# Performance work log

Hardware: AMD Instinct MI355X
Metric: run time of the kernel (lower is better)

## Reference

```python
import math
import jax, jax.numpy as jnp
import numpy as np

EMBED_DIM = 768
NUM_HEADS = 12
HEAD_DIM = EMBED_DIM // NUM_HEADS
NUM_BUCKETS = 32
MAX_DISTANCE = 128
B, S = 8, 1024


def setup_inputs() -> dict:
    key = jax.random.key(0)
    ks = jax.random.split(key, 16)
    sc = 0.02
    d = {
        "query": jax.random.normal(ks[0], (B, S, EMBED_DIM), jnp.float32),
        "Wq": jax.random.normal(ks[1], (EMBED_DIM, EMBED_DIM), jnp.float32) * sc,
        "bq": jnp.zeros((EMBED_DIM,), jnp.float32),
        "Wk": jax.random.normal(ks[2], (EMBED_DIM, EMBED_DIM), jnp.float32) * sc,
        "bk": jnp.zeros((EMBED_DIM,), jnp.float32),
        "Wv": jax.random.normal(ks[3], (EMBED_DIM, EMBED_DIM), jnp.float32) * sc,
        "bv": jnp.zeros((EMBED_DIM,), jnp.float32),
        "Wo": jax.random.normal(ks[4], (EMBED_DIM, EMBED_DIM), jnp.float32) * sc,
        "bo": jnp.zeros((EMBED_DIM,), jnp.float32),
        "rel_embed": jax.random.normal(ks[5], (NUM_BUCKETS, NUM_HEADS), jnp.float32) * sc,
        "gru_W": jax.random.normal(ks[6], (HEAD_DIM, 8), jnp.float32) * sc,
        "gru_b": jnp.zeros((8,), jnp.float32),
        "gru_const": jnp.ones((1, NUM_HEADS, 1, 1), jnp.float32),
    }
    return d


def _rel_pos_bias(rel_embed, seq_len):
    # bidirectional T5-style bucketing, matching WavLM._relative_positions_bucket
    ctx = jnp.arange(seq_len)[:, None]
    mem = jnp.arange(seq_len)[None, :]
    rp = mem - ctx  # [S, S]
    nb = NUM_BUCKETS // 2
    buckets = (rp > 0).astype(jnp.int32) * nb
    arp = jnp.abs(rp)
    max_exact = nb // 2
    is_small = arp < max_exact
    # truncation toward zero == astype for positive values; clamp to avoid log(0)
    large = max_exact + (
        jnp.log(jnp.maximum(arp, 1).astype(jnp.float32) / max_exact)
        / math.log(MAX_DISTANCE / max_exact)
        * (nb - max_exact)
    ).astype(jnp.int32)
    large = jnp.minimum(large, nb - 1)
    buckets = buckets + jnp.where(is_small, arp, large)
    # embedding lookup -> [S, S, H] -> [H, S, S]
    return rel_embed[buckets].transpose(2, 0, 1)


def reference(query, Wq, bq, Wk, bk, Wv, bv, Wo, bo, rel_embed, gru_W, gru_b, gru_const):
    b, s, e = query.shape
    h, d = NUM_HEADS, HEAD_DIM
    pos_bias = _rel_pos_bias(rel_embed, s)  # [H, S, S]

    # GRU-style gate computed from raw query, per head
    ql = query.reshape(b, s, h, d).transpose(0, 2, 1, 3)  # [B, H, S, D]
    g = jax.nn.sigmoid((ql @ gru_W + gru_b).reshape(b, h, s, 2, 4).sum(-1))  # [B,H,S,2]
    gate_a = g[..., 0:1]
    gate_b = g[..., 1:2]
    gate = gate_a * (gate_b * gru_const - 1.0) + 2.0  # [B, H, S, 1]
    attn_mask = gate * pos_bias[None]  # [B, H, S, S]

    scale = d ** (-0.5)
    q = (query @ Wq + bq).reshape(b, s, h, d).transpose(0, 2, 1, 3) * scale
    k = (query @ Wk + bk).reshape(b, s, h, d).transpose(0, 2, 1, 3)
    v = (query @ Wv + bv).reshape(b, s, h, d).transpose(0, 2, 1, 3)

    scores = jnp.einsum("bhqd,bhkd->bhqk", q, k) + attn_mask
    w = jax.nn.softmax(scores, axis=-1)  # max-subtraction in torch is a no-op math-wise
    out = jnp.einsum("bhqk,bhkd->bhqd", w, v)
    out = out.transpose(0, 2, 1, 3).reshape(b, s, h * d)
    return out @ Wo + bo
```

## Files before the change

kernel.cpp:

```cpp
#include <hip/hip_runtime.h>
#include <hip/hip_bf16.h>
#include <math.h>

#define EMBED 768
#define NH 12
#define HD 64
#define SEQ 1024
#define BATCH 8
#define NROWS (BATCH * SEQ)
#define LOG2E 1.44269504088896340736f

typedef __attribute__((ext_vector_type(4))) float f32x4;
typedef __attribute__((ext_vector_type(8))) short short8;
typedef __attribute__((ext_vector_type(8))) _Float16 half8;
typedef unsigned short u16;

__device__ __forceinline__ u16 f2bf(float x) {
    union { float f; unsigned u; } v; v.f = x;
    unsigned r = v.u + 0x7fff + ((v.u >> 16) & 1);
    return (u16)(r >> 16);
}
__device__ __forceinline__ void split2h(float x, u16& hi, u16& lo) {
    _Float16 h = (_Float16)x;
    _Float16 l = (_Float16)(x - (float)h);
    union { _Float16 f; u16 u; } a, b;
    a.f = h; b.f = l;
    hi = a.u; lo = b.u;
}
__device__ __forceinline__ u16 f2h(float x) {
    union { _Float16 f; u16 u; } a; a.f = (_Float16)x; return a.u;
}
__device__ __forceinline__ unsigned pkbf(float a, float b) {
    union { __hip_bfloat162 v; unsigned u; } cv;
    cv.v = __float22bfloat162_rn(make_float2(a, b));
    return cv.u;
}
__device__ __forceinline__ void gll16(const void* g, void* l) {
    __builtin_amdgcn_global_load_lds(
        (const __attribute__((address_space(1))) unsigned int*)g,
        (__attribute__((address_space(3))) unsigned int*)l,
        16, 0, 0);
}
__device__ __forceinline__ void pipe_barrier() {
    asm volatile("s_waitcnt vmcnt(0)" ::: "memory");
    __builtin_amdgcn_s_barrier();
    asm volatile("" ::: "memory");
}

__global__ void bias_table_kernel(const float* __restrict__ rel_embed,
                                  float* __restrict__ bt)
{
    int idx = blockIdx.x * 256 + threadIdx.x;
    const int total = NH * 2047;
    if (idx >= total) return;
    int h    = idx / 2047;
    int dpos = idx - h * 2047;
    int rp   = dpos - 1023;
    int bucket = (rp > 0) ? 16 : 0;
    int arp = rp < 0 ? -rp : rp;
    if (arp < 8) {
        bucket += arp;
    } else {
        double v = log((double)arp / 8.0) / log(16.0) * 8.0;
        int l = 8 + (int)v;
        if (l > 15) l = 15;
        bucket += l;
    }
    bt[idx] = rel_embed[bucket * NH + h] * LOG2E;
}

__global__ void gate_kernel(const float* __restrict__ query,
                            const float* __restrict__ gru_W,
                            const float* __restrict__ gru_b,
                            const float* __restrict__ gru_c,
                            float* __restrict__ gate)
{
    int idx = blockIdx.x * 256 + threadIdx.x;
    if (idx >= BATCH * NH * SEQ) return;
    int s  = idx & (SEQ - 1);
    int bh = idx >> 10;
    int h  = bh % NH;
    int b  = bh / NH;

    const float* x = query + ((size_t)(b * SEQ + s) * EMBED + h * HD);
    float z[8] = {0.f, 0.f, 0.f, 0.f, 0.f, 0.f, 0.f, 0.f};
    for (int d = 0; d < HD; ++d) {
        float xv = x[d];
        const float* wrow = gru_W + d * 8;
        #pragma unroll
        for (int c = 0; c < 8; ++c) z[c] += xv * wrow[c];
    }
    float s0 = (z[0] + gru_b[0]) + (z[1] + gru_b[1]) + (z[2] + gru_b[2]) + (z[3] + gru_b[3]);
    float s1 = (z[4] + gru_b[4]) + (z[5] + gru_b[5]) + (z[6] + gru_b[6]) + (z[7] + gru_b[7]);
    float g0 = 1.f / (1.f + expf(-s0));
    float g1 = 1.f / (1.f + expf(-s1));
    gate[idx] = g0 * (g1 * gru_c[h] - 1.f) + 2.f;
}

__global__ __launch_bounds__(256)
void convertA_h(const float* __restrict__ A, u16* __restrict__ Ah,
                u16* __restrict__ Al)
{
    int idx = (blockIdx.x * 256 + threadIdx.x) * 4;
    float4 v = *(const float4*)(A + idx);
    ushort4 h, l;
    split2h(v.x, h.x, l.x); split2h(v.y, h.y, l.y);
    split2h(v.z, h.z, l.z); split2h(v.w, h.w, l.w);
    *(ushort4*)(Ah + idx) = h;
    *(ushort4*)(Al + idx) = l;
}

__global__ __launch_bounds__(256)
void convertWT4(const float* __restrict__ W0, const float* __restrict__ W1,
                const float* __restrict__ W2, const float* __restrict__ W3,
                u16* __restrict__ T0, u16* __restrict__ T1,
                u16* __restrict__ T2, u16* __restrict__ T3)
{
    __shared__ float tile[32][33];
    const float* W = (blockIdx.z == 0) ? W0 : (blockIdx.z == 1) ? W1
                   : (blockIdx.z == 2) ? W2 : W3;
    u16* WT        = (blockIdx.z == 0) ? T0 : (blockIdx.z == 1) ? T1
                   : (blockIdx.z == 2) ? T2 : T3;
    int t  = threadIdx.x;
    int k0 = blockIdx.y * 32, n0 = blockIdx.x * 32;
    int r = t >> 3, c = (t & 7) * 4;
    float4 v = *(const float4*)&W[(size_t)(k0 + r) * EMBED + n0 + c];
    tile[r][c] = v.x; tile[r][c + 1] = v.y; tile[r][c + 2] = v.z; tile[r][c + 3] = v.w;
    __syncthreads();
    int n = t >> 3, ks = (t & 7) * 4;
    ushort4 h;
    h.x = f2h(tile[ks    ][n]);
    h.y = f2h(tile[ks + 1][n]);
    h.z = f2h(tile[ks + 2][n]);
    h.w = f2h(tile[ks + 3][n]);
    *(ushort4*)&WT[(size_t)(n0 + n) * EMBED + k0 + ks] = h;
}

__global__ __launch_bounds__(256, 3)
void gemm_qkv_p(const u16* __restrict__ Ah, const u16* __restrict__ Al,
                const u16* __restrict__ WqT, const u16* __restrict__ WkT,
                const u16* __restrict__ WvT,
                const float* __restrict__ bq, const float* __restrict__ bk,
                const float* __restrict__ bv,
                u16* __restrict__ Qb, u16* __restrict__ Kb, u16* __restrict__ VT,
                float qscale)
{
    __shared__ u16 Bs[2][3][128 * 32];

    const int t    = threadIdx.x;
    const int lane = t & 63;
    const int wid  = t >> 6;
    const int L    = lane & 15;
    const int quad = lane >> 4;
    const int row0 = blockIdx.y * 32;
    const int col0 = blockIdx.x * 128;
    const int wm   = (wid >> 1) * 16;
    const int wn   = (wid & 1) * 64;

    f32x4 accQ[4], accK[4], accV[4];
    #pragma unroll
    for (int nt = 0; nt < 4; ++nt) {
        accQ[nt] = (f32x4){0.f, 0.f, 0.f, 0.f};
        accK[nt] = (f32x4){0.f, 0.f, 0.f, 0.f};
        accV[nt] = (f32x4){0.f, 0.f, 0.f, 0.f};
    }

    const int rB = t >> 2;
    const int cB = (t & 3) ^ (rB & 3);
    const size_t bo0 = (size_t)(col0 + rB) * EMBED + 8 * cB;
    const size_t bo1 = (size_t)(col0 + 64 + rB) * EMBED + 8 * cB;

    const u16* ApH = Ah + (size_t)(row0 + wm + L) * EMBED + quad * 8;
    const u16* ApL = Al + (size_t)(row0 + wm + L) * EMBED + quad * 8;

    const int swz = 8 * (quad ^ (L & 3));

    {
        char* base = (char*)Bs + wid * 1024;
        gll16(WqT + bo0, base);             gll16(WqT + bo1, base + 4096);
        gll16(WkT + bo0, base + 8192);      gll16(WkT + bo1, base + 12288);
        gll16(WvT + bo0, base + 16384);     gll16(WvT + bo1, base + 20480);
    }
    half8 ah = *(const half8*)ApH;
    half8 al = *(const half8*)ApL;

    int cur = 0;
    for (int k0 = 0; k0 < EMBED; k0 += 32, cur ^= 1) {
        pipe_barrier();

        half8 ahn, aln;
        if (k0 + 32 < EMBED) {
            char* base = (char*)Bs + (cur ^ 1) * 24576 + wid * 1024;
            gll16(WqT + bo0 + k0 + 32, base);         gll16(WqT + bo1 + k0 + 32, base + 4096);
            gll16(WkT + bo0 + k0 + 32, base + 8192);  gll16(WkT + bo1 + k0 + 32, base + 12288);
            gll16(WvT + bo0 + k0 + 32, base + 16384); gll16(WvT + bo1 + k0 + 32, base + 20480);
            ahn = *(const half8*)(ApH + k0 + 32);
            aln = *(const half8*)(ApL + k0 + 32);
        }

        const u16* Bq = &Bs[cur][0][0];
        const u16* Bk = &Bs[cur][1][0];
        const u16* Bv = &Bs[cur][2][0];
        #pragma unroll
        for (int nt = 0; nt < 4; ++nt) {
            const int boff = (wn + nt * 16 + L) * 32 + swz;
            half8 b0 = *(const half8*)&Bq[boff];
            accQ[nt] = __builtin_amdgcn_mfma_f32_16x16x32_f16(ah, b0, accQ[nt], 0, 0, 0);
            accQ[nt] = __builtin_amdgcn_mfma_f32_16x16x32_f16(al, b0, accQ[nt], 0, 0, 0);
            half8 b1 = *(const half8*)&Bk[boff];
            accK[nt] = __builtin_amdgcn_mfma_f32_16x16x32_f16(ah, b1, accK[nt], 0, 0, 0);
            accK[nt] = __builtin_amdgcn_mfma_f32_16x16x32_f16(al, b1, accK[nt], 0, 0, 0);
            half8 b2 = *(const half8*)&Bv[boff];
            accV[nt] = __builtin_amdgcn_mfma_f32_16x16x32_f16(ah, b2, accV[nt], 0, 0, 0);
            accV[nt] = __builtin_amdgcn_mfma_f32_16x16x32_f16(al, b2, accV[nt], 0, 0, 0);
        }
        ah = ahn; al = aln;
    }

    float bq4[4], bk4[4], bv4[4];
    #pragma unroll
    for (int nt = 0; nt < 4; ++nt) {
        int n = col0 + wn + nt * 16 + L;
        bq4[nt] = bq[n]; bk4[nt] = bk[n]; bv4[nt] = bv[n];
    }

    const int rowa = row0 + wm + quad * 4;
    #pragma unroll
    for (int r = 0; r < 4; ++r) {
        size_t base = (size_t)(rowa + r) * EMBED + col0 + wn + L;
        #pragma unroll
        for (int nt = 0; nt < 4; ++nt) {
            Qb[base + nt * 16] = f2bf((accQ[nt][r] + bq4[nt]) * qscale);
            Kb[base + nt * 16] = f2bf(accK[nt][r] + bk4[nt]);
        }
    }
    {
        int b_  = rowa >> 10;
        int s0_ = rowa & 1023;
        #pragma unroll
        for (int nt = 0; nt < 4; ++nt) {
            int n = col0 + wn + nt * 16 + L;
            int hh = n >> 6, dd = n & 63;
            ushort4 pk;
            pk.x = f2bf(accV[nt][0] + bv4[nt]);
            pk.y = f2bf(accV[nt][1] + bv4[nt]);
            pk.z = f2bf(accV[nt][2] + bv4[nt]);
            pk.w = f2bf(accV[nt][3] + bv4[nt]);
            *(ushort4*)&VT[((size_t)(b_ * NH + hh) * HD + dd) * SEQ + s0_] = pk;
        }
    }
}

__global__ __launch_bounds__(256, 3)
void gemm_out_p(const u16* __restrict__ Ah, const u16* __restrict__ Al,
                const u16* __restrict__ BT, const float* __restrict__ bias,
                float* __restrict__ C)
{
    __shared__ u16 Bs[2][128 * 32];

    const int t    = threadIdx.x;
    const int lane = t & 63;
    const int wid  = t >> 6;
    const int L    = lane & 15;
    const int quad = lane >> 4;
    const int row0 = blockIdx.y * 64;
    const int col0 = blockIdx.x * 128;
    const int wm   = (wid >> 1) * 32;
    const int wn   = (wid & 1) * 64;

    f32x4 acc[2][4];
    #pragma unroll
    for (int mt = 0; mt < 2; ++mt)
        #pragma unroll
        for (int nt = 0; nt < 4; ++nt) acc[mt][nt] = (f32x4){0.f, 0.f, 0.f, 0.f};

    const int rB = t >> 2;
    const int cB = (t & 3) ^ (rB & 3);
    const size_t bo0 = (size_t)(col0 + rB) * EMBED + 8 * cB;
    const size_t bo1 = (size_t)(col0 + 64 + rB) * EMBED + 8 * cB;

    const u16* ApH[2]; const u16* ApL[2];
    #pragma unroll
    for (int mt = 0; mt < 2; ++mt) {
        ApH[mt] = Ah + (size_t)(row0 + wm + mt * 16 + L) * EMBED + quad * 8;
        ApL[mt] = Al + (size_t)(row0 + wm + mt * 16 + L) * EMBED + quad * 8;
    }

    const int swz = 8 * (quad ^ (L & 3));

    {
        char* base = (char*)Bs + wid * 1024;
        gll16(BT + bo0, base);
        gll16(BT + bo1, base + 4096);
    }
    half8 ah[2], al[2];
    #pragma unroll
    for (int mt = 0; mt < 2; ++mt) {
        ah[mt] = *(const half8*)ApH[mt];
        al[mt] = *(const half8*)ApL[mt];
    }

    int cur = 0;
    for (int k0 = 0; k0 < EMBED; k0 += 32, cur ^= 1) {
        pipe_barrier();

        half8 ahn[2], aln[2];
        if (k0 + 32 < EMBED) {
            char* base = (char*)Bs + (cur ^ 1) * 8192 + wid * 1024;
            gll16(BT + bo0 + k0 + 32, base);
            gll16(BT + bo1 + k0 + 32, base + 4096);
            #pragma unroll
            for (int mt = 0; mt < 2; ++mt) {
                ahn[mt] = *(const half8*)(ApH[mt] + k0 + 32);
                aln[mt] = *(const half8*)(ApL[mt] + k0 + 32);
            }
        }

        const u16* B = &Bs[cur][0];
        #pragma unroll
        for (int nt = 0; nt < 4; ++nt) {
            half8 b = *(const half8*)&B[(wn + nt * 16 + L) * 32 + swz];
            #pragma unroll
            for (int mt = 0; mt < 2; ++mt) {
                acc[mt][nt] = __builtin_amdgcn_mfma_f32_16x16x32_f16(ah[mt], b, acc[mt][nt], 0, 0, 0);
                acc[mt][nt] = __builtin_amdgcn_mfma_f32_16x16x32_f16(al[mt], b, acc[mt][nt], 0, 0, 0);
            }
        }
        #pragma unroll
        for (int mt = 0; mt < 2; ++mt) { ah[mt] = ahn[mt]; al[mt] = aln[mt]; }
    }

    float b4[4];
    #pragma unroll
    for (int nt = 0; nt < 4; ++nt) b4[nt] = bias[col0 + wn + nt * 16 + L];
    #pragma unroll
    for (int mt = 0; mt < 2; ++mt)
        #pragma unroll
        for (int r = 0; r < 4; ++r) {
            size_t base = (size_t)(row0 + wm + mt * 16 + quad * 4 + r) * EMBED + col0 + wn + L;
            #pragma unroll
            for (int nt = 0; nt < 4; ++nt)
                C[base + nt * 16] = acc[mt][nt][r] + b4[nt];
        }
}

__global__ __launch_bounds__(256)
void attn_mfma3(const u16* __restrict__ Qg, const u16* __restrict__ Kg,
                const u16* __restrict__ VTg, const float* __restrict__ gate,
                const float* __restrict__ bias_tab,
                u16* __restrict__ Oh, u16* __restrict__ Ol)
{
    __shared__ float2   btP[2047];
    __shared__ u16      Klds[64 * 64];
    __shared__ u16      Vlds[64 * 64];
    __shared__ unsigned PB[4][32 * 20];

    const int t    = threadIdx.x;
    const int lane = t & 63;
    const int wid  = t >> 6;
    const int L    = lane & 15;
    const int quad = lane >> 4;

    const int bh = blockIdx.y;
    const int b  = bh / NH;
    const int h  = bh % NH;
    const int qw = blockIdx.x * 128 + wid * 32;

    for (int i = t; i < 2047; i += 256) {
        float a  = bias_tab[h * 2047 + i];
        float nb = (i < 2046) ? bias_tab[h * 2047 + i + 1] : 0.f;
        btP[i] = make_float2(a, nb);
    }

    short8 qf[2][2];
    int   qabs[2];
    float g2[2];
    #pragma unroll
    for (int qt = 0; qt < 2; ++qt) {
        qabs[qt] = qw + qt * 16 + L;
        g2[qt]   = gate[(size_t)bh * SEQ + qabs[qt]];
        const u16* qp = Qg + ((size_t)(b * SEQ + qabs[qt]) * EMBED + h * HD + quad * 8);
        qf[qt][0] = *(const short8*)qp;
        qf[qt][1] = *(const short8*)(qp + 32);
    }

    float lac[2] = {0.f, 0.f};
    f32x4 o[4][2];
    #pragma unroll
    for (int dt = 0; dt < 4; ++dt)
        #pragma unroll
        for (int qt = 0; qt < 2; ++qt) o[dt][qt] = (f32x4){0.f, 0.f, 0.f, 0.f};

    const int k_a = t >> 3, c_a = (t & 7) ^ (k_a & 7);
    const u16* gK0 = Kg + ((size_t)(b * SEQ + k_a) * EMBED + h * HD + 8 * c_a);
    const u16* gK1 = Kg + ((size_t)(b * SEQ + 32 + k_a) * EMBED + h * HD + 8 * c_a);
    char* lK0 = (char*)Klds + wid * 1024;
    char* lK1 = (char*)Klds + 4096 + wid * 1024;

    const int d_a = t >> 3, cv_a = (t & 7) ^ (d_a & 7);
    const u16* gV0 = VTg + ((size_t)(bh * HD + d_a) * SEQ + 8 * cv_a);
    const u16* gV1 = VTg + ((size_t)(bh * HD + 32 + d_a) * SEQ + 8 * cv_a);
    char* lV0 = (char*)Vlds + wid * 1024;
    char* lV1 = (char*)Vlds + 4096 + wid * 1024;

    unsigned* PBw = PB[wid];

    for (int k0 = 0; k0 < SEQ; k0 += 64) {
        __syncthreads();
        gll16(gK0 + (size_t)k0 * EMBED, lK0);
        gll16(gK1 + (size_t)k0 * EMBED, lK1);
        gll16(gV0 + k0, lV0);
        gll16(gV1 + k0, lV1);
        __syncthreads();

        f32x4 st[4][2];
        #pragma unroll
        for (int kt = 0; kt < 4; ++kt)
            #pragma unroll
            for (int qt = 0; qt < 2; ++qt) st[kt][qt] = (f32x4){0.f, 0.f, 0.f, 0.f};
        #pragma unroll
        for (int c = 0; c < 2; ++c) {
            #pragma unroll
            for (int kt = 0; kt < 4; ++kt) {
                int krow = kt * 16 + L;
                short8 kf = *(const short8*)&Klds[krow * 64 + 8 * ((c * 4 + quad) ^ (krow & 7))];
                st[kt][0] = __builtin_amdgcn_mfma_f32_16x16x32_bf16(kf, qf[0][c], st[kt][0], 0, 0, 0);
                st[kt][1] = __builtin_amdgcn_mfma_f32_16x16x32_bf16(kf, qf[1][c], st[kt][1], 0, 0, 0);
            }
        }

        #pragma unroll
        for (int c = 0; c < 2; ++c) {
            #pragma unroll
            for (int kt2 = 0; kt2 < 2; ++kt2) {
                int kt = c * 2 + kt2;
                #pragma unroll
                for (int qt = 0; qt < 2; ++qt) {
                    int bidx = k0 + kt * 16 + quad * 4 - qabs[qt] + 1023;
                    float2 u = btP[bidx];
                    float2 v = btP[bidx + 2];
                    float p0 = __builtin_amdgcn_exp2f(st[kt][qt][0] + g2[qt] * u.x);
                    float p1 = __builtin_amdgcn_exp2f(st[kt][qt][1] + g2[qt] * u.y);
                    float p2 = __builtin_amdgcn_exp2f(st[kt][qt][2] + g2[qt] * v.x);
                    float p3 = __builtin_amdgcn_exp2f(st[kt][qt][3] + g2[qt] * v.y);
                    lac[qt] += (p0 + p1) + (p2 + p3);
                    uint2 w;
                    w.x = pkbf(p0, p1);
                    w.y = pkbf(p2, p3);
                    *(uint2*)&PBw[(qt * 16 + L) * 20 + kt2 * 8 + quad * 2] = w;
                }
            }
            short8 pb[2];
            #pragma unroll
            for (int qt = 0; qt < 2; ++qt) {
                union { uint4 u4; short8 v; } w;
                w.u4 = *(const uint4*)&PBw[(qt * 16 + L) * 20 + quad * 4];
                pb[qt] = w.v;
            }
            #pragma unroll
            for (int dt = 0; dt < 4; ++dt) {
                int drow = dt * 16 + L;
                short8 vf = *(const short8*)&Vlds[drow * 64 + 8 * ((c * 4 + quad) ^ (drow & 7))];
                o[dt][0] = __builtin_amdgcn_mfma_f32_16x16x32_bf16(vf, pb[0], o[dt][0], 0, 0, 0);
                o[dt][1] = __builtin_amdgcn_mfma_f32_16x16x32_bf16(vf, pb[1], o[dt][1], 0, 0, 0);
            }
        }
    }

    #pragma unroll
    for (int qt = 0; qt < 2; ++qt) {
        lac[qt] += __shfl_xor(lac[qt], 16);
        lac[qt] += __shfl_xor(lac[qt], 32);
    }
    #pragma unroll
    for (int qt = 0; qt < 2; ++qt) {
        float inv = 1.f / lac[qt];
        #pragma unroll
        for (int dt = 0; dt < 4; ++dt) {
            ushort4 h4, l4;
            split2h(o[dt][qt][0] * inv, h4.x, l4.x);
            split2h(o[dt][qt][1] * inv, h4.y, l4.y);
            split2h(o[dt][qt][2] * inv, h4.z, l4.z);
            split2h(o[dt][qt][3] * inv, h4.w, l4.w);
            size_t base = (size_t)(b * SEQ + qabs[qt]) * EMBED + h * HD + dt * 16 + quad * 4;
            *(ushort4*)&Oh[base] = h4;
            *(ushort4*)&Ol[base] = l4;
        }
    }
}

extern "C" void kernel_launch(void* const* d_in, const int* in_sizes, int n_in,
                              void* d_out, int out_size, void* d_ws, size_t ws_size,
                              hipStream_t stream)
{
    (void)in_sizes; (void)n_in; (void)out_size; (void)ws_size;
    const float* query = (const float*)d_in[0];
    const float* Wq    = (const float*)d_in[1];
    const float* bq    = (const float*)d_in[2];
    const float* Wk    = (const float*)d_in[3];
    const float* bk    = (const float*)d_in[4];
    const float* Wv    = (const float*)d_in[5];
    const float* bv    = (const float*)d_in[6];
    const float* Wo    = (const float*)d_in[7];
    const float* bo    = (const float*)d_in[8];
    const float* rel   = (const float*)d_in[9];
    const float* gruW  = (const float*)d_in[10];
    const float* gruB  = (const float*)d_in[11];
    const float* gruC  = (const float*)d_in[12];
    float* out = (float*)d_out;

    const size_t NE = (size_t)NROWS * EMBED;
    const size_t WN = (size_t)EMBED * EMBED;
    u16* ws   = (u16*)d_ws;
    u16* Ah   = ws;
    u16* Al   = Ah + NE;
    u16* WqT  = Al + NE;
    u16* WkT  = WqT + WN;
    u16* WvT  = WkT + WN;
    u16* WoT  = WvT + WN;
    u16* Qb   = WoT + WN;
    u16* Kb   = Qb + NE;
    u16* VT   = Kb + NE;
    u16* Ohb  = VT + NE;
    u16* Olb  = Ohb + NE;
    float* gate = (float*)(Olb + NE);
    float* bt   = gate + (size_t)BATCH * NH * SEQ;

    bias_table_kernel<<<(NH * 2047 + 255) / 256, 256, 0, stream>>>(rel, bt);
    gate_kernel<<<(BATCH * NH * SEQ + 255) / 256, 256, 0, stream>>>(query, gruW, gruB, gruC, gate);

    convertA_h<<<NE / 1024, 256, 0, stream>>>(query, Ah, Al);
    convertWT4<<<dim3(EMBED / 32, EMBED / 32, 4), 256, 0, stream>>>(
        Wq, Wk, Wv, Wo, WqT, WkT, WvT, WoT);

    dim3 gq(EMBED / 128, NROWS / 32);
    gemm_qkv_p<<<gq, 256, 0, stream>>>(Ah, Al, WqT, WkT, WvT, bq, bk, bv,
                                       Qb, Kb, VT, 0.125f * LOG2E);

    attn_mfma3<<<dim3(SEQ / 128, BATCH * NH), 256, 0, stream>>>(Qb, Kb, VT, gate, bt, Ohb, Olb);

    dim3 go(EMBED / 128, NROWS / 64);
    gemm_out_p<<<go, 256, 0, stream>>>(Ohb, Olb, WoT, bo, out);
}
```

Measured before the change: 302.8 us.

## Drop split-fp16 low parts and enlarge QKV GEMM tile to 64 rows

Replaces the hi/lo split-fp16 emulation of fp32 with a single fp16 operand for the activations in both the QKV and output projections. This halves the MFMA count and the A-operand traffic, and removes the low-part buffers and their writes from the conversion and attention kernels. The QKV GEMM now computes 64 rows per block (two M-subtiles per wave) so each staged weight tile is reused more. The LDS swizzle pattern also changes. Accuracy drops to plain fp16 inputs, which risks exceeding the tolerance.

Result: faster. 245.3 us (-19.0%).

```diff
diff --git a/kernel.cpp b/kernel.cpp
--- a/kernel.cpp
+++ b/kernel.cpp
@@ -19,13 +19,6 @@
     union { float f; unsigned u; } v; v.f = x;
     unsigned r = v.u + 0x7fff + ((v.u >> 16) & 1);
     return (u16)(r >> 16);
-}
-__device__ __forceinline__ void split2h(float x, u16& hi, u16& lo) {
-    _Float16 h = (_Float16)x;
-    _Float16 l = (_Float16)(x - (float)h);
-    union { _Float16 f; u16 u; } a, b;
-    a.f = h; b.f = l;
-    hi = a.u; lo = b.u;
 }
 __device__ __forceinline__ u16 f2h(float x) {
     union { _Float16 f; u16 u; } a; a.f = (_Float16)x; return a.u;
@@ -98,16 +91,13 @@
 }
 
 __global__ __launch_bounds__(256)
-void convertA_h(const float* __restrict__ A, u16* __restrict__ Ah,
-                u16* __restrict__ Al)
+void convertA1(const float* __restrict__ A, u16* __restrict__ Ah)
 {
     int idx = (blockIdx.x * 256 + threadIdx.x) * 4;
     float4 v = *(const float4*)(A + idx);
-    ushort4 h, l;
-    split2h(v.x, h.x, l.x); split2h(v.y, h.y, l.y);
-    split2h(v.z, h.z, l.z); split2h(v.w, h.w, l.w);
+    ushort4 h;
+    h.x = f2h(v.x); h.y = f2h(v.y); h.z = f2h(v.z); h.w = f2h(v.w);
     *(ushort4*)(Ah + idx) = h;
-    *(ushort4*)(Al + idx) = l;
 }
 
 __global__ __launch_bounds__(256)
@@ -137,7 +127,7 @@
 }
 
 __global__ __launch_bounds__(256, 3)
-void gemm_qkv_p(const u16* __restrict__ Ah, const u16* __restrict__ Al,
+void gemm_qkv_s(const u16* __restrict__ Ah,
                 const u16* __restrict__ WqT, const u16* __restrict__ WkT,
                 const u16* __restrict__ WvT,
                 const float* __restrict__ bq, const float* __restrict__ bk,
@@ -146,117 +136,6 @@
                 float qscale)
 {
     __shared__ u16 Bs[2][3][128 * 32];
-
-    const int t    = threadIdx.x;
-    const int lane = t & 63;
-    const int wid  = t >> 6;
-    const int L    = lane & 15;
-    const int quad = lane >> 4;
-    const int row0 = blockIdx.y * 32;
-    const int col0 = blockIdx.x * 128;
-    const int wm   = (wid >> 1) * 16;
-    const int wn   = (wid & 1) * 64;
-
-    f32x4 accQ[4], accK[4], accV[4];
-    #pragma unroll
-    for (int nt = 0; nt < 4; ++nt) {
-        accQ[nt] = (f32x4){0.f, 0.f, 0.f, 0.f};
-        accK[nt] = (f32x4){0.f, 0.f, 0.f, 0.f};
-        accV[nt] = (f32x4){0.f, 0.f, 0.f, 0.f};
-    }
-
-    const int rB = t >> 2;
-    const int cB = (t & 3) ^ (rB & 3);
-    const size_t bo0 = (size_t)(col0 + rB) * EMBED + 8 * cB;
-    const size_t bo1 = (size_t)(col0 + 64 + rB) * EMBED + 8 * cB;
-
-    const u16* ApH = Ah + (size_t)(row0 + wm + L) * EMBED + quad * 8;
-    const u16* ApL = Al + (size_t)(row0 + wm + L) * EMBED + quad * 8;
-
-    const int swz = 8 * (quad ^ (L & 3));
-
-    {
-        char* base = (char*)Bs + wid * 1024;
-        gll16(WqT + bo0, base);             gll16(WqT + bo1, base + 4096);
-        gll16(WkT + bo0, base + 8192);      gll16(WkT + bo1, base + 12288);
-        gll16(WvT + bo0, base + 16384);     gll16(WvT + bo1, base + 20480);
-    }
-    half8 ah = *(const half8*)ApH;
-    half8 al = *(const half8*)ApL;
-
-    int cur = 0;
-    for (int k0 = 0; k0 < EMBED; k0 += 32, cur ^= 1) {
-        pipe_barrier();
-
-        half8 ahn, aln;
-        if (k0 + 32 < EMBED) {
-            char* base = (char*)Bs + (cur ^ 1) * 24576 + wid * 1024;
-            gll16(WqT + bo0 + k0 + 32, base);         gll16(WqT + bo1 + k0 + 32, base + 4096);
-            gll16(WkT + bo0 + k0 + 32, base + 8192);  gll16(WkT + bo1 + k0 + 32, base + 12288);
-            gll16(WvT + bo0 + k0 + 32, base + 16384); gll16(WvT + bo1 + k0 + 32, base + 20480);
-            ahn = *(const half8*)(ApH + k0 + 32);
-            aln = *(const half8*)(ApL + k0 + 32);
-        }
-
-        const u16* Bq = &Bs[cur][0][0];
-        const u16* Bk = &Bs[cur][1][0];
-        const u16* Bv = &Bs[cur][2][0];
-        #pragma unroll
-        for (int nt = 0; nt < 4; ++nt) {
-            const int boff = (wn + nt * 16 + L) * 32 + swz;
-            half8 b0 = *(const half8*)&Bq[boff];
-            accQ[nt] = __builtin_amdgcn_mfma_f32_16x16x32_f16(ah, b0, accQ[nt], 0, 0, 0);
-            accQ[nt] = __builtin_amdgcn_mfma_f32_16x16x32_f16(al, b0, accQ[nt], 0, 0, 0);
-            half8 b1 = *(const half8*)&Bk[boff];
-            accK[nt] = __builtin_amdgcn_mfma_f32_16x16x32_f16(ah, b1, accK[nt], 0, 0, 0);
-            accK[nt] = __builtin_amdgcn_mfma_f32_16x16x32_f16(al, b1, accK[nt], 0, 0, 0);
-            half8 b2 = *(const half8*)&Bv[boff];
-            accV[nt] = __builtin_amdgcn_mfma_f32_16x16x32_f16(ah, b2, accV[nt], 0, 0, 0);
-            accV[nt] = __builtin_amdgcn_mfma_f32_16x16x32_f16(al, b2, accV[nt], 0, 0, 0);
-        }
-        ah = ahn; al = aln;
-    }
-
-    float bq4[4], bk4[4], bv4[4];
-    #pragma unroll
-    for (int nt = 0; nt < 4; ++nt) {
-        int n = col0 + wn + nt * 16 + L;
-        bq4[nt] = bq[n]; bk4[nt] = bk[n]; bv4[nt] = bv[n];
-    }
-
-    const int rowa = row0 + wm + quad * 4;
-    #pragma unroll
-    for (int r = 0; r < 4; ++r) {
-        size_t base = (size_t)(rowa + r) * EMBED + col0 + wn + L;
-        #pragma unroll
-        for (int nt = 0; nt < 4; ++nt) {
-            Qb[base + nt * 16] = f2bf((accQ[nt][r] + bq4[nt]) * qscale);
-            Kb[base + nt * 16] = f2bf(accK[nt][r] + bk4[nt]);
-        }
-    }
-    {
-        int b_  = rowa >> 10;
-        int s0_ = rowa & 1023;
-        #pragma unroll
-        for (int nt = 0; nt < 4; ++nt) {
-            int n = col0 + wn + nt * 16 + L;
-            int hh = n >> 6, dd = n & 63;
-            ushort4 pk;
-            pk.x = f2bf(accV[nt][0] + bv4[nt]);
-            pk.y = f2bf(accV[nt][1] + bv4[nt]);
-            pk.z = f2bf(accV[nt][2] + bv4[nt]);
-            pk.w = f2bf(accV[nt][3] + bv4[nt]);
-            *(ushort4*)&VT[((size_t)(b_ * NH + hh) * HD + dd) * SEQ + s0_] = pk;
-        }
-    }
-}
-
-__global__ __launch_bounds__(256, 3)
-void gemm_out_p(const u16* __restrict__ Ah, const u16* __restrict__ Al,
-                const u16* __restrict__ BT, const float* __restrict__ bias,
-                float* __restrict__ C)
-{
-    __shared__ u16 Bs[2][128 * 32];
 
     const int t    = threadIdx.x;
     const int lane = t & 63;
@@ -268,52 +147,163 @@
     const int wm   = (wid >> 1) * 32;
     const int wn   = (wid & 1) * 64;
 
-    f32x4 acc[2][4];
+    f32x4 accQ[2][4], accK[2][4], accV[2][4];
     #pragma unroll
     for (int mt = 0; mt < 2; ++mt)
         #pragma unroll
-        for (int nt = 0; nt < 4; ++nt) acc[mt][nt] = (f32x4){0.f, 0.f, 0.f, 0.f};
+        for (int nt = 0; nt < 4; ++nt) {
+            accQ[mt][nt] = (f32x4){0.f, 0.f, 0.f, 0.f};
+            accK[mt][nt] = (f32x4){0.f, 0.f, 0.f, 0.f};
+            accV[mt][nt] = (f32x4){0.f, 0.f, 0.f, 0.f};
+        }
 
     const int rB = t >> 2;
-    const int cB = (t & 3) ^ (rB & 3);
+    const int cB = (t & 3) ^ ((rB >> 1) & 3);
     const size_t bo0 = (size_t)(col0 + rB) * EMBED + 8 * cB;
     const size_t bo1 = (size_t)(col0 + 64 + rB) * EMBED + 8 * cB;
 
-    const u16* ApH[2]; const u16* ApL[2];
+    const u16* ApH[2];
+    #pragma unroll
+    for (int mt = 0; mt < 2; ++mt)
+        ApH[mt] = Ah + (size_t)(row0 + wm + mt * 16 + L) * EMBED + quad * 8;
+
+    const int swz = 8 * (quad ^ ((L >> 1) & 3));
+
+    {
+        char* base = (char*)Bs + wid * 1024;
+        gll16(WqT + bo0, base);             gll16(WqT + bo1, base + 4096);
+        gll16(WkT + bo0, base + 8192);      gll16(WkT + bo1, base + 12288);
+        gll16(WvT + bo0, base + 16384);     gll16(WvT + bo1, base + 20480);
+    }
+    half8 ah[2];
+    #pragma unroll
+    for (int mt = 0; mt < 2; ++mt) ah[mt] = *(const half8*)ApH[mt];
+
+    int cur = 0;
+    for (int k0 = 0; k0 < EMBED; k0 += 32, cur ^= 1) {
+        pipe_barrier();
+
+        half8 ahn[2];
+        if (k0 + 32 < EMBED) {
+            char* base = (char*)Bs + (cur ^ 1) * 24576 + wid * 1024;
+            gll16(WqT + bo0 + k0 + 32, base);         gll16(WqT + bo1 + k0 + 32, base + 4096);
+            gll16(WkT + bo0 + k0 + 32, base + 8192);  gll16(WkT + bo1 + k0 + 32, base + 12288);
+            gll16(WvT + bo0 + k0 + 32, base + 16384); gll16(WvT + bo1 + k0 + 32, base + 20480);
+            #pragma unroll
+            for (int mt = 0; mt < 2; ++mt) ahn[mt] = *(const half8*)(ApH[mt] + k0 + 32);
+        }
+
+        const u16* Bq = &Bs[cur][0][0];
+        const u16* Bk = &Bs[cur][1][0];
+        const u16* Bv = &Bs[cur][2][0];
+        #pragma unroll
+        for (int nt = 0; nt < 4; ++nt) {
+            const int boff = (wn + nt * 16 + L) * 32 + swz;
+            half8 b0 = *(const half8*)&Bq[boff];
+            accQ[0][nt] = __builtin_amdgcn_mfma_f32_16x16x32_f16(ah[0], b0, accQ[0][nt], 0, 0, 0);
+            accQ[1][nt] = __builtin_amdgcn_mfma_f32_16x16x32_f16(ah[1], b0, accQ[1][nt], 0, 0, 0);
+            half8 b1 = *(const half8*)&Bk[boff];
+            accK[0][nt] = __builtin_amdgcn_mfma_f32_16x16x32_f16(ah[0], b1, accK[0][nt], 0, 0, 0);
+            accK[1][nt] = __builtin_amdgcn_mfma_f32_16x16x32_f16(ah[1], b1, accK[1][nt], 0, 0, 0);
+            half8 b2 = *(const half8*)&Bv[boff];
+            accV[0][nt] = __builtin_amdgcn_mfma_f32_16x16x32_f16(ah[0], b2, accV[0][nt], 0, 0, 0);
+            accV[1][nt] = __builtin_amdgcn_mfma_f32_16x16x32_f16(ah[1], b2, accV[1][nt], 0, 0, 0);
+        }
+        #pragma unroll
+        for (int mt = 0; mt < 2; ++mt) ah[mt] = ahn[mt];
+    }
+
+    float bq4[4], bk4[4], bv4[4];
+    #pragma unroll
+    for (int nt = 0; nt < 4; ++nt) {
+        int n = col0 + wn + nt * 16 + L;
+        bq4[nt] = bq[n]; bk4[nt] = bk[n]; bv4[nt] = bv[n];
+    }
+
     #pragma unroll
     for (int mt = 0; mt < 2; ++mt) {
+        const int rowa = row0 + wm + mt * 16 + quad * 4;
+        #pragma unroll
+        for (int r = 0; r < 4; ++r) {
+            size_t base = (size_t)(rowa + r) * EMBED + col0 + wn + L;
+            #pragma unroll
+            for (int nt = 0; nt < 4; ++nt) {
+                Qb[base + nt * 16] = f2bf((accQ[mt][nt][r] + bq4[nt]) * qscale);
+                Kb[base + nt * 16] = f2bf(accK[mt][nt][r] + bk4[nt]);
+            }
+        }
+        {
+            int b_  = rowa >> 10;
+            int s0_ = rowa & 1023;
+            #pragma unroll
+            for (int nt = 0; nt < 4; ++nt) {
+                int n = col0 + wn + nt * 16 + L;
+                int hh = n >> 6, dd = n & 63;
+                ushort4 pk;
+                pk.x = f2bf(accV[mt][nt][0] + bv4[nt]);
+                pk.y = f2bf(accV[mt][nt][1] + bv4[nt]);
+                pk.z = f2bf(accV[mt][nt][2] + bv4[nt]);
+                pk.w = f2bf(accV[mt][nt][3] + bv4[nt]);
+                *(ushort4*)&VT[((size_t)(b_ * NH + hh) * HD + dd) * SEQ + s0_] = pk;
+            }
+        }
+    }
+}
+
+__global__ __launch_bounds__(256, 3)
+void gemm_out_s(const u16* __restrict__ Ah, const u16* __restrict__ BT,
+                const float* __restrict__ bias, float* __restrict__ C)
+{
+    __shared__ u16 Bs[2][128 * 32];
+
+    const int t    = threadIdx.x;
+    const int lane = t & 63;
+    const int wid  = t >> 6;
+    const int L    = lane & 15;
+    const int quad = lane >> 4;
+    const int row0 = blockIdx.y * 64;
+    const int col0 = blockIdx.x * 128;
+    const int wm   = (wid >> 1) * 32;
+    const int wn   = (wid & 1) * 64;
+
+    f32x4 acc[2][4];
+    #pragma unroll
+    for (int mt = 0; mt < 2; ++mt)
+        #pragma unroll
+        for (int nt = 0; nt < 4; ++nt) acc[mt][nt] = (f32x4){0.f, 0.f, 0.f, 0.f};
+
+    const int rB = t >> 2;
+    const int cB = (t & 3) ^ ((rB >> 1) & 3);
+    const size_t bo0 = (size_t)(col0 + rB) * EMBED + 8 * cB;
+    const size_t bo1 = (size_t)(col0 + 64 + rB) * EMBED + 8 * cB;
+
+    const u16* ApH[2];
+    #pragma unroll
+    for (int mt = 0; mt < 2; ++mt)
         ApH[mt] = Ah + (size_t)(row0 + wm + mt * 16 + L) * EMBED + quad * 8;
-        ApL[mt] = Al + (size_t)(row0 + wm + mt * 16 + L) * EMBED + quad * 8;
-    }
-
-    const int swz = 8 * (quad ^ (L & 3));
+
+    const int swz = 8 * (quad ^ ((L >> 1) & 3));
 
     {
         char* base = (char*)Bs + wid * 1024;
         gll16(BT + bo0, base);
         gll16(BT + bo1, base + 4096);
     }
-    half8 ah[2], al[2];
-    #pragma unroll
-    for (int mt = 0; mt < 2; ++mt) {
-        ah[mt] = *(const half8*)ApH[mt];
-        al[mt] = *(const half8*)ApL[mt];
-    }
+    half8 ah[2];
+    #pragma unroll
+    for (int mt = 0; mt < 2; ++mt) ah[mt] = *(const half8*)ApH[mt];
 
     int cur = 0;
     for (int k0 = 0; k0 < EMBED; k0 += 32, cur ^= 1) {
         pipe_barrier();
 
-        half8 ahn[2], aln[2];
+        half8 ahn[2];
         if (k0 + 32 < EMBED) {
             char* base = (char*)Bs + (cur ^ 1) * 8192 + wid * 1024;
             gll16(BT + bo0 + k0 + 32, base);
             gll16(BT + bo1 + k0 + 32, base + 4096);
             #pragma unroll
-            for (int mt = 0; mt < 2; ++mt) {
-                ahn[mt] = *(const half8*)(ApH[mt] + k0 + 32);
-                aln[mt] = *(const half8*)(ApL[mt] + k0 + 32);
-            }
+            for (int mt = 0; mt < 2; ++mt) ahn[mt] = *(const half8*)(ApH[mt] + k0 + 32);
         }
 
         const u16* B = &Bs[cur][0];
@@ -321,13 +311,11 @@
         for (int nt = 0; nt < 4; ++nt) {
             half8 b = *(const half8*)&B[(wn + nt * 16 + L) * 32 + swz];
             #pragma unroll
-            for (int mt = 0; mt < 2; ++mt) {
+            for (int mt = 0; mt < 2; ++mt)
                 acc[mt][nt] = __builtin_amdgcn_mfma_f32_16x16x32_f16(ah[mt], b, acc[mt][nt], 0, 0, 0);
-                acc[mt][nt] = __builtin_amdgcn_mfma_f32_16x16x32_f16(al[mt], b, acc[mt][nt], 0, 0, 0);
-            }
-        }
-        #pragma unroll
-        for (int mt = 0; mt < 2; ++mt) { ah[mt] = ahn[mt]; al[mt] = aln[mt]; }
+        }
+        #pragma unroll
+        for (int mt = 0; mt < 2; ++mt) ah[mt] = ahn[mt];
     }
 
     float b4[4];
@@ -348,7 +336,7 @@
 void attn_mfma3(const u16* __restrict__ Qg, const u16* __restrict__ Kg,
                 const u16* __restrict__ VTg, const float* __restrict__ gate,
                 const float* __restrict__ bias_tab,
-                u16* __restrict__ Oh, u16* __restrict__ Ol)
+                u16* __restrict__ Oh)
 {
     __shared__ float2   btP[2047];
     __shared__ u16      Klds[64 * 64];
@@ -477,14 +465,13 @@
         float inv = 1.f / lac[qt];
         #pragma unroll
         for (int dt = 0; dt < 4; ++dt) {
-            ushort4 h4, l4;
-            split2h(o[dt][qt][0] * inv, h4.x, l4.x);
-            split2h(o[dt][qt][1] * inv, h4.y, l4.y);
-            split2h(o[dt][qt][2] * inv, h4.z, l4.z);
-            split2h(o[dt][qt][3] * inv, h4.w, l4.w);
+            ushort4 h4;
+            h4.x = f2h(o[dt][qt][0] * inv);
+            h4.y = f2h(o[dt][qt][1] * inv);
+            h4.z = f2h(o[dt][qt][2] * inv);
+            h4.w = f2h(o[dt][qt][3] * inv);
             size_t base = (size_t)(b * SEQ + qabs[qt]) * EMBED + h * HD + dt * 16 + quad * 4;
             *(ushort4*)&Oh[base] = h4;
-            *(ushort4*)&Ol[base] = l4;
         }
     }
 }
@@ -513,32 +500,29 @@
     const size_t WN = (size_t)EMBED * EMBED;
     u16* ws   = (u16*)d_ws;
     u16* Ah   = ws;
-    u16* Al   = Ah + NE;
-    u16* WqT  = Al + NE;
+    u16* WqT  = Ah + NE;
     u16* WkT  = WqT + WN;
     u16* WvT  = WkT + WN;
     u16* WoT  = WvT + WN;
     u16* Qb   = WoT + WN;
     u16* Kb   = Qb + NE;
     u16* VT   = Kb + NE;
-    u16* Ohb  = VT + NE;
-    u16* Olb  = Ohb + NE;
-    float* gate = (float*)(Olb + NE);
+    u16* Ohh  = VT + NE;
+    float* gate = (float*)(Ohh + NE);
     float* bt   = gate + (size_t)BATCH * NH * SEQ;
 
     bias_table_kernel<<<(NH * 2047 + 255) / 256, 256, 0, stream>>>(rel, bt);
     gate_kernel<<<(BATCH * NH * SEQ + 255) / 256, 256, 0, stream>>>(query, gruW, gruB, gruC, gate);
 
-    convertA_h<<<NE / 1024, 256, 0, stream>>>(query, Ah, Al);
+    convertA1<<<NE / 1024, 256, 0, stream>>>(query, Ah);
     convertWT4<<<dim3(EMBED / 32, EMBED / 32, 4), 256, 0, stream>>>(
         Wq, Wk, Wv, Wo, WqT, WkT, WvT, WoT);
 
-    dim3 gq(EMBED / 128, NROWS / 32);
-    gemm_qkv_p<<<gq, 256, 0, stream>>>(Ah, Al, WqT, WkT, WvT, bq, bk, bv,
+    dim3 gg(EMBED / 128, NROWS / 64);
+    gemm_qkv_s<<<gg, 256, 0, stream>>>(Ah, WqT, WkT, WvT, bq, bk, bv,
                                        Qb, Kb, VT, 0.125f * LOG2E);
 
-    attn_mfma3<<<dim3(SEQ / 128, BATCH * NH), 256, 0, stream>>>(Qb, Kb, VT, gate, bt, Ohb, Olb);
-
-    dim3 go(EMBED / 128, NROWS / 64);
-    gemm_out_p<<<go, 256, 0, stream>>>(Ohb, Olb, WoT, bo, out);
-}
+    attn_mfma3<<<dim3(SEQ / 128, BATCH * NH), 256, 0, stream>>>(Qb, Kb, VT, gate, bt, Ohh);
+
+    gemm_out_s<<<gg, 256, 0, stream>>>(Ohh, WoT, bo, out);
+}
```
